# Optimization experiments

Measured on AMD Instinct MI355X. Metric: run time of the kernel, lower is better.

## Reference

```python
import jax, jax.numpy as jnp
import numpy as np

# mamba-2.8b layer dims
B_, L = 2, 2048
D_MODEL = 2560
D_IN = 2 * D_MODEL          # 5120, d_inner
N = 16                      # d_state
DT_RANK = D_MODEL // 16     # 160


def setup_inputs() -> dict:
    key = jax.random.key(0)
    ks = jax.random.split(key, 6)
    x = jax.random.normal(ks[0], (B_, L, D_IN), dtype=jnp.float32)
    # A_log initialized so A = -exp(A_log) in [-16, -1], as in Mamba's S4D-real init
    A_log = jnp.log(jax.random.uniform(ks[1], (D_IN, N), minval=1.0, maxval=16.0, dtype=jnp.float32))
    D = jax.random.normal(ks[2], (D_IN,), dtype=jnp.float32) * 0.1 + 1.0
    x_proj_w = jax.random.normal(ks[3], (DT_RANK + 2 * N, D_IN), dtype=jnp.float32) * (D_IN ** -0.5)
    dt_proj_w = jax.random.normal(ks[4], (D_IN, DT_RANK), dtype=jnp.float32) * (DT_RANK ** -0.5)
    dt_proj_b = jax.random.normal(ks[5], (D_IN,), dtype=jnp.float32) * 0.1
    return {"x": x, "A_log": A_log, "D": D, "x_proj_w": x_proj_w,
            "dt_proj_w": dt_proj_w, "dt_proj_b": dt_proj_b}


def _ssm(x, A_log, D, x_proj_w, dt_proj_w, dt_proj_b):
    # x: (b, l, d_inner)
    A = -jnp.exp(A_log)                                        # (d, n)
    x_dbl = jnp.einsum('bld,ed->ble', x, x_proj_w)             # (b, l, dt_rank+2n)
    dt_raw = x_dbl[..., :DT_RANK]                              # (b, l, dt_rank)
    Bm = x_dbl[..., DT_RANK:DT_RANK + N]                       # (b, l, n)
    Cm = x_dbl[..., DT_RANK + N:]                              # (b, l, n)
    delta = jax.nn.softplus(jnp.einsum('blr,dr->bld', dt_raw, dt_proj_w) + dt_proj_b)  # (b, l, d)

    def step(h, inp):
        xt, dt, Bt, Ct = inp                                   # (b,d) (b,d) (b,n) (b,n)
        dA = jnp.exp(dt[..., None] * A)                        # (b, d, n)
        h = dA * h + (dt * xt)[..., None] * Bt[:, None, :]     # (b, d, n)
        y = jnp.einsum('bdn,bn->bd', h, Ct)                    # (b, d)
        return h, y

    xs = (jnp.swapaxes(x, 0, 1), jnp.swapaxes(delta, 0, 1),
          jnp.swapaxes(Bm, 0, 1), jnp.swapaxes(Cm, 0, 1))
    h0 = jnp.zeros((x.shape[0], D_IN, N), dtype=x.dtype)
    _, ys = jax.lax.scan(step, h0, xs)                         # ys: (l, b, d)
    return jnp.swapaxes(ys, 0, 1) + x * D                      # (b, l, d)


def reference(x, A_log, D, x_proj_w, dt_proj_w, dt_proj_b):
    return _ssm(x, A_log, D, x_proj_w, dt_proj_w, dt_proj_b)
```

## Files before the change

kernel.cpp:

```cpp
#include <hip/hip_runtime.h>
#include <hip/hip_bf16.h>

#define DIN   5120
#define LSEQ  2048
#define BATCH 2
#define MROWS 4096
#define EOUT  192
#define RDT   160
#define NST   16
#define NC    32
#define LC    64
#define LOG2E 1.44269504088896f
#define LN2   0.69314718055995f

typedef __attribute__((ext_vector_type(8))) short bf16x8;
typedef __attribute__((ext_vector_type(4))) float f32x4;

__device__ __forceinline__ void stdelta(float* p, size_t i, float v) { p[i] = v; }
__device__ __forceinline__ void stdelta(__hip_bfloat16* p, size_t i, float v) { p[i] = __float2bfloat16(v); }
__device__ __forceinline__ float lddelta(const float* p, size_t i) { return p[i]; }
__device__ __forceinline__ float lddelta(const __hip_bfloat16* p, size_t i) { return __bfloat162float(p[i]); }

__device__ __forceinline__ float softplus_fast(float v) {
    float t = __builtin_amdgcn_exp2f(-fabsf(v) * LOG2E);
    return fmaxf(v, 0.f) + __builtin_amdgcn_logf(1.f + t) * LN2;
}
__device__ __forceinline__ unsigned short bf16rne(float f) {
    unsigned int u = __float_as_uint(f);
    unsigned int r = (u + 0x7FFFu + ((u >> 16) & 1u)) >> 16;
    return (unsigned short)r;
}
__device__ __forceinline__ void cvt8(float4 a, float4 b, bf16x8& h, bf16x8& l) {
    float v[8] = {a.x, a.y, a.z, a.w, b.x, b.y, b.z, b.w};
    #pragma unroll
    for (int e = 0; e < 8; e++) {
        unsigned int u = __float_as_uint(v[e]);
        unsigned int hb = u & 0xFFFF0000u;
        h[e] = (short)(hb >> 16);
        l[e] = (short)bf16rne(v[e] - __uint_as_float(hb));
    }
}

__global__ void k0_cvtw(const float* __restrict__ w, ushort* __restrict__ bw) {
    int i = blockIdx.x * 256 + threadIdx.x;
    float4 v = reinterpret_cast<const float4*>(w)[i];
    ushort4 o = make_ushort4(bf16rne(v.x), bf16rne(v.y), bf16rne(v.z), bf16rne(v.w));
    reinterpret_cast<ushort4*>(bw)[i] = o;
}

template <int KPS>
__global__ __launch_bounds__(256) void k1_mfma(const float* __restrict__ x,
                                               const ushort* __restrict__ bWp,
                                               float* __restrict__ part) {
    const int tid = threadIdx.x;
    const int m_base = blockIdx.x * 128;
    const int k_base = blockIdx.y * KPS;
    const int lane = tid & 63, w = tid >> 6;
    const int lr = lane & 15, lg = lane >> 4;
    const int wm = m_base + w * 32;

    f32x4 acc[2][12];
    #pragma unroll
    for (int i = 0; i < 2; i++)
        #pragma unroll
        for (int j = 0; j < 12; j++) acc[i][j] = (f32x4)(0.f);

    const float* xr0 = x + (size_t)(wm + lr) * DIN + k_base;
    const float* xr1 = x + (size_t)(wm + 16 + lr) * DIN + k_base;

    #pragma unroll 2
    for (int kk = 0; kk < KPS / 32; kk++) {
        const int ko = kk * 32 + lg * 8;
        float4 v0 = *reinterpret_cast<const float4*>(xr0 + ko);
        float4 v1 = *reinterpret_cast<const float4*>(xr0 + ko + 4);
        float4 v2 = *reinterpret_cast<const float4*>(xr1 + ko);
        float4 v3 = *reinterpret_cast<const float4*>(xr1 + ko + 4);
        bf16x8 ah0, al0, ah1, al1;
        cvt8(v0, v1, ah0, al0);
        cvt8(v2, v3, ah1, al1);
        #pragma unroll
        for (int j = 0; j < 12; j++) {
            bf16x8 bb = *reinterpret_cast<const bf16x8*>(bWp + (size_t)(j * 16 + lr) * DIN + k_base + ko);
            acc[0][j] = __builtin_amdgcn_mfma_f32_16x16x32_bf16(ah0, bb, acc[0][j], 0, 0, 0);
            acc[1][j] = __builtin_amdgcn_mfma_f32_16x16x32_bf16(ah1, bb, acc[1][j], 0, 0, 0);
            acc[0][j] = __builtin_amdgcn_mfma_f32_16x16x32_bf16(al0, bb, acc[0][j], 0, 0, 0);
            acc[1][j] = __builtin_amdgcn_mfma_f32_16x16x32_bf16(al1, bb, acc[1][j], 0, 0, 0);
        }
    }
    float* p = part + (size_t)blockIdx.y * MROWS * EOUT;
    #pragma unroll
    for (int j = 0; j < 12; j++) {
        const int e = j * 16 + lr;
        #pragma unroll
        for (int i = 0; i < 2; i++) {
            const int m0 = wm + i * 16 + lg * 4;
            #pragma unroll
            for (int r = 0; r < 4; r++)
                p[(size_t)(m0 + r) * EOUT + e] = acc[i][j][r];
        }
    }
}

template <int KS>
__global__ void k1_reduce(const float* __restrict__ part, float* __restrict__ xdbl,
                          ushort* __restrict__ aHi, ushort* __restrict__ aLo) {
    int i = blockIdx.x * 256 + threadIdx.x;
    const float4* p = reinterpret_cast<const float4*>(part);
    float4 s = p[i];
    #pragma unroll
    for (int k = 1; k < KS; k++) {
        float4 v = p[(size_t)k * (MROWS * EOUT / 4) + i];
        s.x += v.x; s.y += v.y; s.z += v.z; s.w += v.w;
    }
    reinterpret_cast<float4*>(xdbl)[i] = s;
    int row = i / 48, e4 = i % 48;
    if (e4 < 40) {
        unsigned int hx = __float_as_uint(s.x) & 0xFFFF0000u;
        unsigned int hy = __float_as_uint(s.y) & 0xFFFF0000u;
        unsigned int hz = __float_as_uint(s.z) & 0xFFFF0000u;
        unsigned int hw = __float_as_uint(s.w) & 0xFFFF0000u;
        ushort4 hv = make_ushort4((unsigned short)(hx >> 16), (unsigned short)(hy >> 16),
                                  (unsigned short)(hz >> 16), (unsigned short)(hw >> 16));
        ushort4 lv = make_ushort4(bf16rne(s.x - __uint_as_float(hx)),
                                  bf16rne(s.y - __uint_as_float(hy)),
                                  bf16rne(s.z - __uint_as_float(hz)),
                                  bf16rne(s.w - __uint_as_float(hw)));
        *reinterpret_cast<ushort4*>(&aHi[(size_t)row * RDT + e4 * 4]) = hv;
        *reinterpret_cast<ushort4*>(&aLo[(size_t)row * RDT + e4 * 4]) = lv;
    }
}

template <typename DT>
__global__ __launch_bounds__(256, 3) void k2_mfma(const ushort* __restrict__ aHi,
                                                  const ushort* __restrict__ aLo,
                                                  const ushort* __restrict__ bW,
                                                  const float* __restrict__ bias,
                                                  DT* __restrict__ delta) {
    const int tid = threadIdx.x;
    const int m_base = blockIdx.x * 64, d_base = blockIdx.y * 256;
    const int lane = tid & 63, w = tid >> 6;
    const int wr = w >> 1, wc = w & 1;
    const int lr = lane & 15, lg = lane >> 4;

    f32x4 acc[2][8];
    #pragma unroll
    for (int i = 0; i < 2; i++)
        #pragma unroll
        for (int j = 0; j < 8; j++) acc[i][j] = (f32x4)(0.f);

    const size_t arow = (size_t)(m_base + wr * 32 + lr) * RDT;
    const size_t brow = (size_t)(d_base + wc * 128 + lr) * RDT;

    #pragma unroll
    for (int kk = 0; kk < 5; kk++) {
        const int ko = kk * 32 + lg * 8;
        bf16x8 ah0 = *reinterpret_cast<const bf16x8*>(aHi + arow + ko);
        bf16x8 ah1 = *reinterpret_cast<const bf16x8*>(aHi + arow + 16 * RDT + ko);
        bf16x8 al0 = *reinterpret_cast<const bf16x8*>(aLo + arow + ko);
        bf16x8 al1 = *reinterpret_cast<const bf16x8*>(aLo + arow + 16 * RDT + ko);
        #pragma unroll
        for (int j = 0; j < 8; j++) {
            bf16x8 bb = *reinterpret_cast<const bf16x8*>(bW + brow + (size_t)j * 16 * RDT + ko);
            acc[0][j] = __builtin_amdgcn_mfma_f32_16x16x32_bf16(ah0, bb, acc[0][j], 0, 0, 0);
            acc[1][j] = __builtin_amdgcn_mfma_f32_16x16x32_bf16(ah1, bb, acc[1][j], 0, 0, 0);
            acc[0][j] = __builtin_amdgcn_mfma_f32_16x16x32_bf16(al0, bb, acc[0][j], 0, 0, 0);
            acc[1][j] = __builtin_amdgcn_mfma_f32_16x16x32_bf16(al1, bb, acc[1][j], 0, 0, 0);
        }
    }

    #pragma unroll
    for (int j = 0; j < 8; j++) {
        const int gd = d_base + wc * 128 + j * 16 + lr;
        const float bv = bias[gd];
        #pragma unroll
        for (int i = 0; i < 2; i++) {
            const int gm0 = m_base + wr * 32 + i * 16 + lg * 4;
            #pragma unroll
            for (int r = 0; r < 4; r++) {
                float v = acc[i][j][r] + bv;
                stdelta(delta, (size_t)(gm0 + r) * DIN + gd, softplus_fast(v));
            }
        }
    }
}

template <typename DT>
__global__ __launch_bounds__(256) void k3a_local(const float* __restrict__ x,
                                                 const DT* __restrict__ delta,
                                                 const float* __restrict__ xdbl,
                                                 const float* __restrict__ A_log,
                                                 float* __restrict__ Sbuf,
                                                 float* __restrict__ hend0) {
    const int tid = threadIdx.x;
    const int d = blockIdx.x * 256 + tid;
    const int c = blockIdx.y, b = blockIdx.z;

    float4 aq[4];
    #pragma unroll
    for (int q = 0; q < 4; q++) aq[q] = *reinterpret_cast<const float4*>(&A_log[d * NST + q * 4]);
    const float* av = reinterpret_cast<const float*>(aq);
    float A2[NST];
    #pragma unroll
    for (int n = 0; n < NST; n++) A2[n] = -expf(av[n]) * LOG2E;

    float h[NST];
    #pragma unroll
    for (int n = 0; n < NST; n++) h[n] = 0.f;
    float S = 0.f;

    const size_t gbase = (size_t)b * LSEQ * DIN + (size_t)c * LC * DIN + d;
    const float* Bbase = xdbl + ((size_t)b * LSEQ + (size_t)c * LC) * EOUT + RDT;

    float dv = lddelta(delta, gbase);
    float xv = x[gbase];
    float4 bq[4];
    {
        const float4* Bp = reinterpret_cast<const float4*>(Bbase);
        bq[0] = Bp[0]; bq[1] = Bp[1]; bq[2] = Bp[2]; bq[3] = Bp[3];
    }
    for (int tt = 0; tt < LC; tt++) {
        const int ttn = (tt + 1 < LC) ? tt + 1 : tt;
        float dv_n = lddelta(delta, gbase + (size_t)ttn * DIN);
        float xv_n = x[gbase + (size_t)ttn * DIN];
        float4 bqn[4];
        {
            const float4* Bp = reinterpret_cast<const float4*>(Bbase + (size_t)ttn * EOUT);
            bqn[0] = Bp[0]; bqn[1] = Bp[1]; bqn[2] = Bp[2]; bqn[3] = Bp[3];
        }
        const float* Bv = reinterpret_cast<const float*>(bq);
        S += dv;
        const float dvx = dv * xv;
        #pragma unroll
        for (int n = 0; n < NST; n++)
            h[n] = fmaf(__builtin_amdgcn_exp2f(dv * A2[n]), h[n], dvx * Bv[n]);
        dv = dv_n; xv = xv_n;
        bq[0] = bqn[0]; bq[1] = bqn[1]; bq[2] = bqn[2]; bq[3] = bqn[3];
    }
    Sbuf[((size_t)b * NC + c) * DIN + d] = S;
    float* hp = hend0 + (((size_t)b * NC + c) * DIN + d) * NST;
    #pragma unroll
    for (int q = 0; q < 4; q++)
        reinterpret_cast<float4*>(hp)[q] = make_float4(h[q*4], h[q*4+1], h[q*4+2], h[q*4+3]);
}

__global__ __launch_bounds__(256) void k3b_combine(const float* __restrict__ Sbuf,
                                                   const float* __restrict__ hend0,
                                                   const float* __restrict__ A_log,
                                                   float* __restrict__ hinit) {
    const int i = blockIdx.x * 256 + threadIdx.x;
    const int b = i / (DIN * NST);
    const int r = i % (DIN * NST);
    const int d = r >> 4;
    const float A2 = -expf(A_log[r]) * LOG2E;
    float hi = 0.f;
    for (int c = 0; c < NC; c++) {
        const size_t idx = ((size_t)b * NC + c) * DIN * NST + r;
        hinit[idx] = hi;
        hi = fmaf(__builtin_amdgcn_exp2f(Sbuf[((size_t)b * NC + c) * DIN + d] * A2), hi, hend0[idx]);
    }
}

template <typename DT>
__global__ __launch_bounds__(256) void k3c_scan(const float* __restrict__ x,
                                                const DT* __restrict__ delta,
                                                const float* __restrict__ xdbl,
                                                const float* __restrict__ A_log,
                                                const float* __restrict__ Dw,
                                                const float* __restrict__ hinit,
                                                float* __restrict__ out) {
    const int tid = threadIdx.x;
    const int d = blockIdx.x * 256 + tid;
    const int c = blockIdx.y, b = blockIdx.z;

    float4 aq[4];
    #pragma unroll
    for (int q = 0; q < 4; q++) aq[q] = *reinterpret_cast<const float4*>(&A_log[d * NST + q * 4]);
    const float* av = reinterpret_cast<const float*>(aq);
    float A2[NST];
    #pragma unroll
    for (int n = 0; n < NST; n++) A2[n] = -expf(av[n]) * LOG2E;

    float h[NST];
    {
        const float* hp = hinit + (((size_t)b * NC + c) * DIN + d) * NST;
        float4 hq[4];
        #pragma unroll
        for (int q = 0; q < 4; q++) hq[q] = reinterpret_cast<const float4*>(hp)[q];
        const float* hv = reinterpret_cast<const float*>(hq);
        #pragma unroll
        for (int n = 0; n < NST; n++) h[n] = hv[n];
    }
    const float Dv = Dw[d];

    const size_t gbase = (size_t)b * LSEQ * DIN + (size_t)c * LC * DIN + d;
    const float* Bbase = xdbl + ((size_t)b * LSEQ + (size_t)c * LC) * EOUT + RDT;

    float dv = lddelta(delta, gbase);
    float xv = x[gbase];
    float4 bq[4], cq[4];
    {
        const float4* Bp = reinterpret_cast<const float4*>(Bbase);
        bq[0] = Bp[0]; bq[1] = Bp[1]; bq[2] = Bp[2]; bq[3] = Bp[3];
        cq[0] = Bp[4]; cq[1] = Bp[5]; cq[2] = Bp[6]; cq[3] = Bp[7];
    }
    for (int tt = 0; tt < LC; tt++) {
        const int ttn = (tt + 1 < LC) ? tt + 1 : tt;
        float dv_n = lddelta(delta, gbase + (size_t)ttn * DIN);
        float xv_n = x[gbase + (size_t)ttn * DIN];
        float4 bqn[4], cqn[4];
        {
            const float4* Bp = reinterpret_cast<const float4*>(Bbase + (size_t)ttn * EOUT);
            bqn[0] = Bp[0]; bqn[1] = Bp[1]; bqn[2] = Bp[2]; bqn[3] = Bp[3];
            cqn[0] = Bp[4]; cqn[1] = Bp[5]; cqn[2] = Bp[6]; cqn[3] = Bp[7];
        }
        const float* Bv = reinterpret_cast<const float*>(bq);
        const float* Cv = reinterpret_cast<const float*>(cq);
        const float dvx = dv * xv;
        float y0 = 0.f, y1 = 0.f, y2 = 0.f, y3 = 0.f;
        #pragma unroll
        for (int n = 0; n < NST; n += 4) {
            h[n+0] = fmaf(__builtin_amdgcn_exp2f(dv * A2[n+0]), h[n+0], dvx * Bv[n+0]);
            y0 = fmaf(h[n+0], Cv[n+0], y0);
            h[n+1] = fmaf(__builtin_amdgcn_exp2f(dv * A2[n+1]), h[n+1], dvx * Bv[n+1]);
            y1 = fmaf(h[n+1], Cv[n+1], y1);
            h[n+2] = fmaf(__builtin_amdgcn_exp2f(dv * A2[n+2]), h[n+2], dvx * Bv[n+2]);
            y2 = fmaf(h[n+2], Cv[n+2], y2);
            h[n+3] = fmaf(__builtin_amdgcn_exp2f(dv * A2[n+3]), h[n+3], dvx * Bv[n+3]);
            y3 = fmaf(h[n+3], Cv[n+3], y3);
        }
        out[gbase + (size_t)tt * DIN] = ((y0 + y1) + (y2 + y3)) + xv * Dv;
        dv = dv_n; xv = xv_n;
        bq[0] = bqn[0]; bq[1] = bqn[1]; bq[2] = bqn[2]; bq[3] = bqn[3];
        cq[0] = cqn[0]; cq[1] = cqn[1]; cq[2] = cqn[2]; cq[3] = cqn[3];
    }
}

extern "C" void kernel_launch(void* const* d_in, const int* in_sizes, int n_in,
                              void* d_out, int out_size, void* d_ws, size_t ws_size,
                              hipStream_t stream) {
    const float* x     = (const float*)d_in[0];
    const float* A_log = (const float*)d_in[1];
    const float* Dw    = (const float*)d_in[2];
    const float* xpw   = (const float*)d_in[3];
    const float* dtw   = (const float*)d_in[4];
    const float* dtb   = (const float*)d_in[5];
    float* out = (float*)d_out;

    char* ws = (char*)d_ws;
    size_t off = 0;
    float* xdbl  = (float*)(ws + off); off += (size_t)MROWS * EOUT * 4;
    float* hend0 = (float*)(ws + off); off += (size_t)BATCH * NC * DIN * NST * 4;
    float* hinit = (float*)(ws + off); off += (size_t)BATCH * NC * DIN * NST * 4;
    float* Sbuf  = (float*)(ws + off); off += (size_t)BATCH * NC * DIN * 4;
    ushort* aHi  = (ushort*)(ws + off); off += (size_t)MROWS * RDT * 2;
    ushort* aLo  = (ushort*)(ws + off); off += (size_t)MROWS * RDT * 2;
    ushort* bW   = (ushort*)(ws + off); off += (size_t)DIN * RDT * 2;
    ushort* bWp  = (ushort*)(ws + off); off += (size_t)EOUT * DIN * 2;
    const size_t delta_off = off;
    const bool f32ok = ws_size >= delta_off + (size_t)MROWS * DIN * 4;

    k0_cvtw<<<dim3(EOUT * DIN / 4 / 256), 256, 0, stream>>>(xpw, bWp);
    k0_cvtw<<<dim3(DIN * RDT / 4 / 256), 256, 0, stream>>>(dtw, bW);

    if (f32ok) {
        float* part = (float*)(ws + delta_off);
        float* delta = (float*)(ws + delta_off);
        k1_mfma<DIN / 16><<<dim3(MROWS / 128, 16), 256, 0, stream>>>(x, bWp, part);
        k1_reduce<16><<<dim3(MROWS * EOUT / 4 / 256), 256, 0, stream>>>(part, xdbl, aHi, aLo);
        k2_mfma<float><<<dim3(MROWS / 64, DIN / 256), 256, 0, stream>>>(aHi, aLo, bW, dtb, delta);
        k3a_local<float><<<dim3(DIN / 256, NC, BATCH), 256, 0, stream>>>(x, delta, xdbl, A_log, Sbuf, hend0);
        k3b_combine<<<dim3(BATCH * DIN * NST / 256), 256, 0, stream>>>(Sbuf, hend0, A_log, hinit);
        k3c_scan<float><<<dim3(DIN / 256, NC, BATCH), 256, 0, stream>>>(x, delta, xdbl, A_log, Dw, hinit, out);
    } else {
        float* part = hend0;
        __hip_bfloat16* delta = (__hip_bfloat16*)(ws + delta_off);
        k1_mfma<DIN / 8><<<dim3(MROWS / 128, 8), 256, 0, stream>>>(x, bWp, part);
        k1_reduce<8><<<dim3(MROWS * EOUT / 4 / 256), 256, 0, stream>>>(part, xdbl, aHi, aLo);
        k2_mfma<__hip_bfloat16><<<dim3(MROWS / 64, DIN / 256), 256, 0, stream>>>(aHi, aLo, bW, dtb, delta);
        k3a_local<__hip_bfloat16><<<dim3(DIN / 256, NC, BATCH), 256, 0, stream>>>(x, delta, xdbl, A_log, Sbuf, hend0);
        k3b_combine<<<dim3(BATCH * DIN * NST / 256), 256, 0, stream>>>(Sbuf, hend0, A_log, hinit);
        k3c_scan<__hip_bfloat16><<<dim3(DIN / 256, NC, BATCH), 256, 0, stream>>>(x, delta, xdbl, A_log, Dw, hinit, out);
    }
}
```

Before: 241.0 us.

## Use more shorter scan chunks and combine chunk states in place

The chunked selective scan now uses 64 chunks of 32 steps instead of 32 chunks of 64. This doubles the blocks available to the local and final scan kernels and halves each thread's serial chain. The combine kernel now handles four states per thread with float4 loads and overwrites the chunk-end states with the chunk-initial states in one buffer, so the separate hinit buffer goes away. In exchange the combine pass has a longer serial chain over chunks with fewer threads, and the per-chunk state traffic is doubled.

After: 238.7 us. Within noise of the previous version (-0.9%).

```diff
diff --git a/kernel.cpp b/kernel.cpp
--- a/kernel.cpp
+++ b/kernel.cpp
@@ -8,8 +8,8 @@
 #define EOUT  192
 #define RDT   160
 #define NST   16
-#define NC    32
-#define LC    64
+#define NC    64
+#define LC    32
 #define LOG2E 1.44269504088896f
 #define LN2   0.69314718055995f
 
@@ -190,7 +190,7 @@
                                                  const float* __restrict__ xdbl,
                                                  const float* __restrict__ A_log,
                                                  float* __restrict__ Sbuf,
-                                                 float* __restrict__ hend0) {
+                                                 float* __restrict__ hboth) {
     const int tid = threadIdx.x;
     const int d = blockIdx.x * 256 + tid;
     const int c = blockIdx.y, b = blockIdx.z;
@@ -237,26 +237,33 @@
         bq[0] = bqn[0]; bq[1] = bqn[1]; bq[2] = bqn[2]; bq[3] = bqn[3];
     }
     Sbuf[((size_t)b * NC + c) * DIN + d] = S;
-    float* hp = hend0 + (((size_t)b * NC + c) * DIN + d) * NST;
+    float* hp = hboth + (((size_t)b * NC + c) * DIN + d) * NST;
     #pragma unroll
     for (int q = 0; q < 4; q++)
         reinterpret_cast<float4*>(hp)[q] = make_float4(h[q*4], h[q*4+1], h[q*4+2], h[q*4+3]);
 }
 
 __global__ __launch_bounds__(256) void k3b_combine(const float* __restrict__ Sbuf,
-                                                   const float* __restrict__ hend0,
-                                                   const float* __restrict__ A_log,
-                                                   float* __restrict__ hinit) {
+                                                   float* __restrict__ hboth,
+                                                   const float* __restrict__ A_log) {
     const int i = blockIdx.x * 256 + threadIdx.x;
-    const int b = i / (DIN * NST);
-    const int r = i % (DIN * NST);
-    const int d = r >> 4;
-    const float A2 = -expf(A_log[r]) * LOG2E;
-    float hi = 0.f;
+    const int b = i / (DIN * 4);
+    const int r = i % (DIN * 4);
+    const int d = r >> 2, q = r & 3;
+    float4 av = *reinterpret_cast<const float4*>(&A_log[d * NST + q * 4]);
+    float A2x = -expf(av.x) * LOG2E, A2y = -expf(av.y) * LOG2E;
+    float A2z = -expf(av.z) * LOG2E, A2w = -expf(av.w) * LOG2E;
+    float4 hi = make_float4(0.f, 0.f, 0.f, 0.f);
+    float4* hb4 = reinterpret_cast<float4*>(hboth);
     for (int c = 0; c < NC; c++) {
-        const size_t idx = ((size_t)b * NC + c) * DIN * NST + r;
-        hinit[idx] = hi;
-        hi = fmaf(__builtin_amdgcn_exp2f(Sbuf[((size_t)b * NC + c) * DIN + d] * A2), hi, hend0[idx]);
+        const size_t idx4 = (((size_t)b * NC + c) * DIN + d) * 4 + q;
+        float4 he = hb4[idx4];
+        float S = Sbuf[((size_t)b * NC + c) * DIN + d];
+        hb4[idx4] = hi;
+        hi.x = fmaf(__builtin_amdgcn_exp2f(S * A2x), hi.x, he.x);
+        hi.y = fmaf(__builtin_amdgcn_exp2f(S * A2y), hi.y, he.y);
+        hi.z = fmaf(__builtin_amdgcn_exp2f(S * A2z), hi.z, he.z);
+        hi.w = fmaf(__builtin_amdgcn_exp2f(S * A2w), hi.w, he.w);
     }
 }
 
@@ -266,7 +273,7 @@
                                                 const float* __restrict__ xdbl,
                                                 const float* __restrict__ A_log,
                                                 const float* __restrict__ Dw,
-                                                const float* __restrict__ hinit,
+                                                const float* __restrict__ hboth,
                                                 float* __restrict__ out) {
     const int tid = threadIdx.x;
     const int d = blockIdx.x * 256 + tid;
@@ -282,7 +289,7 @@
 
     float h[NST];
     {
-        const float* hp = hinit + (((size_t)b * NC + c) * DIN + d) * NST;
+        const float* hp = hboth + (((size_t)b * NC + c) * DIN + d) * NST;
         float4 hq[4];
         #pragma unroll
         for (int q = 0; q < 4; q++) hq[q] = reinterpret_cast<const float4*>(hp)[q];
@@ -349,8 +356,7 @@
     char* ws = (char*)d_ws;
     size_t off = 0;
     float* xdbl  = (float*)(ws + off); off += (size_t)MROWS * EOUT * 4;
-    float* hend0 = (float*)(ws + off); off += (size_t)BATCH * NC * DIN * NST * 4;
-    float* hinit = (float*)(ws + off); off += (size_t)BATCH * NC * DIN * NST * 4;
+    float* hboth = (float*)(ws + off); off += (size_t)BATCH * NC * DIN * NST * 4;
     float* Sbuf  = (float*)(ws + off); off += (size_t)BATCH * NC * DIN * 4;
     ushort* aHi  = (ushort*)(ws + off); off += (size_t)MROWS * RDT * 2;
     ushort* aLo  = (ushort*)(ws + off); off += (size_t)MROWS * RDT * 2;
@@ -368,17 +374,17 @@
         k1_mfma<DIN / 16><<<dim3(MROWS / 128, 16), 256, 0, stream>>>(x, bWp, part);
         k1_reduce<16><<<dim3(MROWS * EOUT / 4 / 256), 256, 0, stream>>>(part, xdbl, aHi, aLo);
         k2_mfma<float><<<dim3(MROWS / 64, DIN / 256), 256, 0, stream>>>(aHi, aLo, bW, dtb, delta);
-        k3a_local<float><<<dim3(DIN / 256, NC, BATCH), 256, 0, stream>>>(x, delta, xdbl, A_log, Sbuf, hend0);
-        k3b_combine<<<dim3(BATCH * DIN * NST / 256), 256, 0, stream>>>(Sbuf, hend0, A_log, hinit);
-        k3c_scan<float><<<dim3(DIN / 256, NC, BATCH), 256, 0, stream>>>(x, delta, xdbl, A_log, Dw, hinit, out);
+        k3a_local<float><<<dim3(DIN / 256, NC, BATCH), 256, 0, stream>>>(x, delta, xdbl, A_log, Sbuf, hboth);
+        k3b_combine<<<dim3(BATCH * DIN * 4 / 256), 256, 0, stream>>>(Sbuf, hboth, A_log);
+        k3c_scan<float><<<dim3(DIN / 256, NC, BATCH), 256, 0, stream>>>(x, delta, xdbl, A_log, Dw, hboth, out);
     } else {
-        float* part = hend0;
+        float* part = hboth;
         __hip_bfloat16* delta = (__hip_bfloat16*)(ws + delta_off);
         k1_mfma<DIN / 8><<<dim3(MROWS / 128, 8), 256, 0, stream>>>(x, bWp, part);
         k1_reduce<8><<<dim3(MROWS * EOUT / 4 / 256), 256, 0, stream>>>(part, xdbl, aHi, aLo);
         k2_mfma<__hip_bfloat16><<<dim3(MROWS / 64, DIN / 256), 256, 0, stream>>>(aHi, aLo, bW, dtb, delta);
-        k3a_local<__hip_bfloat16><<<dim3(DIN / 256, NC, BATCH), 256, 0, stream>>>(x, delta, xdbl, A_log, Sbuf, hend0);
-        k3b_combine<<<dim3(BATCH * DIN * NST / 256), 256, 0, stream>>>(Sbuf, hend0, A_log, hinit);
-        k3c_scan<__hip_bfloat16><<<dim3(DIN / 256, NC, BATCH), 256, 0, stream>>>(x, delta, xdbl, A_log, Dw, hinit, out);
-    }
-}
+        k3a_local<__hip_bfloat16><<<dim3(DIN / 256, NC, BATCH), 256, 0, stream>>>(x, delta, xdbl, A_log, Sbuf, hboth);
+        k3b_combine<<<dim3(BATCH * DIN * 4 / 256), 256, 0, stream>>>(Sbuf, hboth, A_log);
+        k3c_scan<__hip_bfloat16><<<dim3(DIN / 256, NC, BATCH), 256, 0, stream>>>(x, delta, xdbl, A_log, Dw, hboth, out);
+    }
+}
```
